# Kernel tuning notes

Measured on AMD Instinct MI355X. Metric: run time of the kernel, lower is better.

The kernel has to match this reference:

```python
import jax, jax.numpy as jnp
import numpy as np

N_NODES = 100000
N_EDGES = 1600000
N_GRAPHS = 4096
IN_DIM, HID, OUT_DIM = 128, 128, 64
BN_EPS = 1e-5


def gcn_conv(x, W, b, src, dst):
    """PyG GCNConv: symmetric norm with self-loops. x:[N,Fin] -> [N,Fout]."""
    h = x @ W  # [N, Fout]
    ones = jnp.ones((src.shape[0],), dtype=h.dtype)
    deg = jax.ops.segment_sum(ones, dst, num_segments=N_NODES) + 1.0  # +1 for self-loop
    dinv = jax.lax.rsqrt(deg)  # deg >= 1, safe
    norm = dinv[src] * dinv[dst]  # [E]
    msg = h[src] * norm[:, None]  # [E, Fout] gather + scale
    agg = jax.ops.segment_sum(msg, dst, num_segments=N_NODES)
    agg = agg + h * (dinv * dinv)[:, None]  # self-loop term, norm = dinv_i^2
    return agg + b


def batchnorm(x, gamma, beta):
    mu = jnp.mean(x, axis=0)
    var = jnp.mean(jnp.square(x - mu), axis=0)  # biased var, torch BN training mode
    return (x - mu) * jax.lax.rsqrt(var + BN_EPS) * gamma + beta


def setup_inputs() -> dict:
    key = jax.random.key(0)
    ks = jax.random.split(key, 12)
    x = jax.random.normal(ks[0], (N_NODES, IN_DIM), dtype=jnp.float32)
    edge_index = jax.random.randint(ks[1], (2, N_EDGES), 0, N_NODES, dtype=jnp.int64)
    batch = jnp.sort(jax.random.randint(ks[2], (N_NODES,), 0, N_GRAPHS, dtype=jnp.int64))
    def lin(k, fi, fo):
        s = 1.0 / np.sqrt(fi)
        return jax.random.uniform(k, (fi, fo), jnp.float32, -s, s)
    return {
        "x": x, "edge_index": edge_index, "batch": batch,
        "W1": lin(ks[3], IN_DIM, HID), "b1": jnp.zeros((HID,), jnp.float32),
        "g1": jnp.ones((HID,), jnp.float32), "be1": jnp.zeros((HID,), jnp.float32),
        "W2": lin(ks[4], HID, HID), "b2": jnp.zeros((HID,), jnp.float32),
        "g2": jnp.ones((HID,), jnp.float32), "be2": jnp.zeros((HID,), jnp.float32),
        "W3": lin(ks[5], HID, HID), "b3": jnp.zeros((HID,), jnp.float32),
        "g3": jnp.ones((HID,), jnp.float32), "be3": jnp.zeros((HID,), jnp.float32),
        "fcW": lin(ks[6], HID, OUT_DIM),
        "fcb": jax.random.uniform(ks[7], (OUT_DIM,), jnp.float32, -1/np.sqrt(HID), 1/np.sqrt(HID)),
    }


def reference(x, edge_index, batch, W1, b1, g1, be1, W2, b2, g2, be2, W3, b3, g3, be3, fcW, fcb):
    src, dst = edge_index[0], edge_index[1]
    h = jax.nn.relu(batchnorm(gcn_conv(x, W1, b1, src, dst), g1, be1))
    h = jax.nn.relu(batchnorm(gcn_conv(h, W2, b2, src, dst), g2, be2))
    h = jax.nn.relu(batchnorm(gcn_conv(h, W3, b3, src, dst), g3, be3))
    # global mean pool over graphs
    sums = jax.ops.segment_sum(h, batch, num_segments=N_GRAPHS)  # [G, HID]
    cnt = jax.ops.segment_sum(jnp.ones((N_NODES,), h.dtype), batch, num_segments=N_GRAPHS)
    pooled = sums / jnp.maximum(cnt, 1.0)[:, None]
    return pooled @ fcW + fcb
```

## Files before the change

kernel.cpp:

```cpp
#include <hip/hip_runtime.h>

#define NN 100000
#define NE 1600000
#define NG 4096
#define HID 128
#define ODIM 64
#define BN_EPS 1e-5f
#define NBUK 782
#define CHUNK 16384

typedef unsigned int u32;
typedef unsigned short u16;
typedef short short8 __attribute__((ext_vector_type(8)));
typedef float f32x4 __attribute__((ext_vector_type(4)));

__device__ inline u32 pack_bf16(float a, float b) {
  u32 ua = __float_as_uint(a), ub = __float_as_uint(b);
  ua += 0x7fffu + ((ua >> 16) & 1u);
  ub += 0x7fffu + ((ub >> 16) & 1u);
  return (ua >> 16) | (ub & 0xffff0000u);
}
__device__ inline u16 bf16_of(float v) {
  u32 ua = __float_as_uint(v);
  ua += 0x7fffu + ((ua >> 16) & 1u);
  return (u16)(ua >> 16);
}
__device__ inline float bf_lo(u32 u) { return __uint_as_float(u << 16); }
__device__ inline float bf_hi(u32 u) { return __uint_as_float(u & 0xffff0000u); }

__global__ __launch_bounds__(256) void k_bhist(const int* __restrict__ ei, int* __restrict__ bcnt) {
  __shared__ int h[NBUK];
  for (int i = threadIdx.x; i < NBUK; i += 256) h[i] = 0;
  __syncthreads();
  const int stride = 256 * 256;
  for (int e = blockIdx.x * 256 + threadIdx.x; e < NE; e += stride)
    atomicAdd(&h[ei[NE + e] >> 7], 1);
  __syncthreads();
  for (int i = threadIdx.x; i < NBUK; i += 256)
    if (h[i]) atomicAdd(&bcnt[i], h[i]);
}

__global__ __launch_bounds__(1024) void k_bscan(const int* __restrict__ bcnt, int* __restrict__ bboff,
                                                int* __restrict__ bcur, int* __restrict__ off) {
  __shared__ int ls[1024];
  int t = threadIdx.x;
  ls[t] = (t < NBUK) ? bcnt[t] : 0;
  __syncthreads();
  for (int d = 1; d < 1024; d <<= 1) {
    int v = 0;
    if (t >= d) v = ls[t - d];
    __syncthreads();
    ls[t] += v;
    __syncthreads();
  }
  if (t < NBUK) {
    int ex = (t == 0) ? 0 : ls[t - 1];
    bboff[t] = ex;
    bcur[t] = ex;
  }
  if (t == 0) { bboff[NBUK] = NE; off[NN] = NE; }
}

__global__ __launch_bounds__(1024) void k_bscatter(const int* __restrict__ ei, int* __restrict__ bcur,
                                                   u32* __restrict__ ebuf) {
  __shared__ int cnt[NBUK], rnk[NBUK], base[NBUK];
  int t = threadIdx.x;
  int e0 = blockIdx.x * CHUNK;
  for (int i = t; i < NBUK; i += 1024) { cnt[i] = 0; rnk[i] = 0; }
  __syncthreads();
  for (int i = t; i < CHUNK; i += 1024) {
    int e = e0 + i;
    if (e < NE) atomicAdd(&cnt[ei[NE + e] >> 7], 1);
  }
  __syncthreads();
  for (int i = t; i < NBUK; i += 1024) {
    int c = cnt[i];
    base[i] = c ? atomicAdd(&bcur[i], c) : 0;
  }
  __syncthreads();
  for (int i = t; i < CHUNK; i += 1024) {
    int e = e0 + i;
    if (e < NE) {
      int s = ei[e], d = ei[NE + e];
      int b = d >> 7;
      int r = atomicAdd(&rnk[b], 1);
      ebuf[base[b] + r] = ((u32)(d & 127) << 17) | (u32)s;
    }
  }
}

__global__ __launch_bounds__(256) void k_csr(const u32* __restrict__ ebuf, const int* __restrict__ bboff,
                                             int* __restrict__ off, float* __restrict__ dinv,
                                             u32* __restrict__ csrc) {
  __shared__ int cnt[128], base[128];
  int b = blockIdx.x, t = threadIdx.x;
  int n0 = b << 7;
  int ebeg = bboff[b], eend = bboff[b + 1];
  if (t < 128) cnt[t] = 0;
  __syncthreads();
  for (int e = ebeg + t; e < eend; e += 256) atomicAdd(&cnt[ebuf[e] >> 17], 1);
  __syncthreads();
  if (t < 128) base[t] = cnt[t];
  __syncthreads();
  for (int d = 1; d < 128; d <<= 1) {
    int v = 0;
    if (t >= d && t < 128) v = base[t - d];
    __syncthreads();
    if (t < 128) base[t] += v;
    __syncthreads();
  }
  int nvalid = min(128, NN - n0);
  if (t < 128) {
    int ex = base[t] - cnt[t];
    base[t] = ex;
    if (t < nvalid) {
      off[n0 + t] = ebeg + ex;
      dinv[n0 + t] = rsqrtf((float)cnt[t] + 1.0f);
    }
  }
  __syncthreads();
  for (int e = ebeg + t; e < eend; e += 256) {
    u32 p = ebuf[e];
    int d = p >> 17;
    int pos = ebeg + atomicAdd(&base[d], 1);
    csrc[pos] = p & 0x1ffffu;
  }
}

__global__ __launch_bounds__(256) void k_goff(const int* __restrict__ batch, int* __restrict__ goff) {
  int g = blockIdx.x * 256 + threadIdx.x;
  if (g > NG) return;
  int lo = 0, hi = NN;
  while (lo < hi) { int mid = (lo + hi) >> 1; if (batch[mid] < g) lo = mid + 1; else hi = mid; }
  goff[g] = lo;
}

__global__ __launch_bounds__(128) void k_wprep(const float* __restrict__ W, u16* __restrict__ Wt) {
  int n = blockIdx.x, k = threadIdx.x;
  Wt[(size_t)n * HID + k] = bf16_of(W[(size_t)k * HID + n]);
}

__global__ __launch_bounds__(256) void k_gemm1(const float* __restrict__ A, const u16* __restrict__ Wt,
                                               const float* __restrict__ dinv, u16* __restrict__ H) {
  __shared__ u16 Ct[128][128];
  u16 (*At)[32] = (u16 (*)[32])(&Ct[0][0]);
  u16 (*Bt)[32] = (u16 (*)[32])(&Ct[32][0]);

  int t = threadIdx.x;
  int w = t >> 6, l = t & 63;
  int quad = l >> 4, lid = l & 15;
  int row0 = blockIdx.x * 128;

  f32x4 acc[2][8];
#pragma unroll
  for (int mt = 0; mt < 2; ++mt)
#pragma unroll
    for (int nt = 0; nt < 8; ++nt) acc[mt][nt] = (f32x4){0.f, 0.f, 0.f, 0.f};

  int ar = t >> 1;
  int ac = (t & 1) << 4;
  int grow = row0 + ar;
  bool aok = grow < NN;

  for (int k0 = 0; k0 < HID; k0 += 32) {
    float4 f0 = {0, 0, 0, 0}, f1 = {0, 0, 0, 0}, f2 = {0, 0, 0, 0}, f3 = {0, 0, 0, 0};
    if (aok) {
      const float4* ap = (const float4*)(A + (size_t)grow * HID + k0 + ac);
      f0 = ap[0]; f1 = ap[1]; f2 = ap[2]; f3 = ap[3];
    }
    uint4 q0, q1;
    q0.x = pack_bf16(f0.x, f0.y); q0.y = pack_bf16(f0.z, f0.w);
    q0.z = pack_bf16(f1.x, f1.y); q0.w = pack_bf16(f1.z, f1.w);
    q1.x = pack_bf16(f2.x, f2.y); q1.y = pack_bf16(f2.z, f2.w);
    q1.z = pack_bf16(f3.x, f3.y); q1.w = pack_bf16(f3.z, f3.w);
    *(uint4*)&At[ar][ac] = q0;
    *(uint4*)&At[ar][ac + 8] = q1;
    const u16* wp = Wt + (size_t)(t >> 1) * HID + k0 + ac;
    *(uint4*)&Bt[t >> 1][ac]     = ((const uint4*)wp)[0];
    *(uint4*)&Bt[t >> 1][ac + 8] = ((const uint4*)wp)[1];
    __syncthreads();
    short8 a0 = *(const short8*)&At[(w << 5) + lid][quad << 3];
    short8 a1 = *(const short8*)&At[(w << 5) + 16 + lid][quad << 3];
#pragma unroll
    for (int nt = 0; nt < 8; ++nt) {
      short8 b = *(const short8*)&Bt[(nt << 4) + lid][quad << 3];
      acc[0][nt] = __builtin_amdgcn_mfma_f32_16x16x32_bf16(a0, b, acc[0][nt], 0, 0, 0);
      acc[1][nt] = __builtin_amdgcn_mfma_f32_16x16x32_bf16(a1, b, acc[1][nt], 0, 0, 0);
    }
    __syncthreads();
  }

  int valid = min(128, NN - row0);
#pragma unroll
  for (int mt = 0; mt < 2; ++mt) {
#pragma unroll
    for (int r = 0; r < 4; ++r) {
      int rl = (w << 5) + (mt << 4) + (quad << 2) + r;
      float dv = (rl < valid) ? dinv[row0 + rl] : 0.f;
#pragma unroll
      for (int nt = 0; nt < 8; ++nt) {
        Ct[rl][(nt << 4) + lid] = bf16_of(acc[mt][nt][r] * dv);
      }
    }
  }
  __syncthreads();
  u16* Hb = H + (size_t)row0 * HID;
  int tot = valid << 4;
  for (int idx = t; idx < tot; idx += 256) {
    ((uint4*)Hb)[idx] = ((const uint4*)Ct)[idx];
  }
}

__device__ inline u32 bn_pair(u32 v, float2 sc, float2 sh) {
  float a = fmaxf(fmaf(bf_lo(v), sc.x, sh.x), 0.f);
  float b = fmaxf(fmaf(bf_hi(v), sc.y, sh.y), 0.f);
  return pack_bf16(a, b);
}

__global__ __launch_bounds__(256) void k_gemm_b(const u16* __restrict__ A, const u16* __restrict__ Wt,
                                                const float* __restrict__ scale, const float* __restrict__ shift,
                                                const float* __restrict__ dinv, u16* __restrict__ H) {
  __shared__ u16 Ct[128][128];
  u16 (*At)[32] = (u16 (*)[32])(&Ct[0][0]);
  u16 (*Bt)[32] = (u16 (*)[32])(&Ct[32][0]);

  int t = threadIdx.x;
  int w = t >> 6, l = t & 63;
  int quad = l >> 4, lid = l & 15;
  int row0 = blockIdx.x * 128;

  f32x4 acc[2][8];
#pragma unroll
  for (int mt = 0; mt < 2; ++mt)
#pragma unroll
    for (int nt = 0; nt < 8; ++nt) acc[mt][nt] = (f32x4){0.f, 0.f, 0.f, 0.f};

  int ar = t >> 1;
  int ac = (t & 1) << 4;
  int grow = row0 + ar;
  bool aok = grow < NN;

  for (int k0 = 0; k0 < HID; k0 += 32) {
    uint4 q0 = {0, 0, 0, 0}, q1 = {0, 0, 0, 0};
    if (aok) {
      const uint4* ap = (const uint4*)(A + (size_t)grow * HID + k0 + ac);
      q0 = ap[0]; q1 = ap[1];
    }
    const float2* scp = (const float2*)(scale + k0 + ac);
    const float2* shp = (const float2*)(shift + k0 + ac);
    q0.x = bn_pair(q0.x, scp[0], shp[0]); q0.y = bn_pair(q0.y, scp[1], shp[1]);
    q0.z = bn_pair(q0.z, scp[2], shp[2]); q0.w = bn_pair(q0.w, scp[3], shp[3]);
    q1.x = bn_pair(q1.x, scp[4], shp[4]); q1.y = bn_pair(q1.y, scp[5], shp[5]);
    q1.z = bn_pair(q1.z, scp[6], shp[6]); q1.w = bn_pair(q1.w, scp[7], shp[7]);
    *(uint4*)&At[ar][ac] = q0;
    *(uint4*)&At[ar][ac + 8] = q1;
    const u16* wp = Wt + (size_t)(t >> 1) * HID + k0 + ac;
    *(uint4*)&Bt[t >> 1][ac]     = ((const uint4*)wp)[0];
    *(uint4*)&Bt[t >> 1][ac + 8] = ((const uint4*)wp)[1];
    __syncthreads();
    short8 a0 = *(const short8*)&At[(w << 5) + lid][quad << 3];
    short8 a1 = *(const short8*)&At[(w << 5) + 16 + lid][quad << 3];
#pragma unroll
    for (int nt = 0; nt < 8; ++nt) {
      short8 b = *(const short8*)&Bt[(nt << 4) + lid][quad << 3];
      acc[0][nt] = __builtin_amdgcn_mfma_f32_16x16x32_bf16(a0, b, acc[0][nt], 0, 0, 0);
      acc[1][nt] = __builtin_amdgcn_mfma_f32_16x16x32_bf16(a1, b, acc[1][nt], 0, 0, 0);
    }
    __syncthreads();
  }

  int valid = min(128, NN - row0);
#pragma unroll
  for (int mt = 0; mt < 2; ++mt) {
#pragma unroll
    for (int r = 0; r < 4; ++r) {
      int rl = (w << 5) + (mt << 4) + (quad << 2) + r;
      float dv = (rl < valid) ? dinv[row0 + rl] : 0.f;
#pragma unroll
      for (int nt = 0; nt < 8; ++nt) {
        Ct[rl][(nt << 4) + lid] = bf16_of(acc[mt][nt][r] * dv);
      }
    }
  }
  __syncthreads();
  u16* Hb = H + (size_t)row0 * HID;
  int tot = valid << 4;
  for (int idx = t; idx < tot; idx += 256) {
    ((uint4*)Hb)[idx] = ((const uint4*)Ct)[idx];
  }
}

__global__ __launch_bounds__(256) void k_agg(const u16* __restrict__ h2, const int* __restrict__ off,
                                             const u32* __restrict__ csrc, const float* __restrict__ dinv,
                                             u16* __restrict__ aggb) {
  int node = (int)((blockIdx.x * 256 + threadIdx.x) >> 6);
  int lane = threadIdx.x & 63;
  if (node >= NN) return;
  int beg = off[node], end = off[node + 1];
  u32 us = ((const u32*)(h2 + (size_t)node * HID))[lane];
  float ax = bf_lo(us), ay = bf_hi(us);
  int e = beg;
  for (; e + 4 <= end; e += 4) {
    u32 s0 = csrc[e], s1 = csrc[e + 1], s2 = csrc[e + 2], s3 = csrc[e + 3];
    u32 v0 = ((const u32*)(h2 + (size_t)s0 * HID))[lane];
    u32 v1 = ((const u32*)(h2 + (size_t)s1 * HID))[lane];
    u32 v2 = ((const u32*)(h2 + (size_t)s2 * HID))[lane];
    u32 v3 = ((const u32*)(h2 + (size_t)s3 * HID))[lane];
    ax += bf_lo(v0) + bf_lo(v1) + bf_lo(v2) + bf_lo(v3);
    ay += bf_hi(v0) + bf_hi(v1) + bf_hi(v2) + bf_hi(v3);
  }
  for (; e < end; ++e) {
    u32 v = ((const u32*)(h2 + (size_t)csrc[e] * HID))[lane];
    ax += bf_lo(v);
    ay += bf_hi(v);
  }
  float di = dinv[node];
  ((u32*)(aggb + (size_t)node * HID))[lane] = pack_bf16(ax * di, ay * di);
}

__global__ __launch_bounds__(256) void k_bnstats(const u16* __restrict__ X, float* __restrict__ buf) {
  __shared__ float lsx[256], lssx[256], lsy[256], lssy[256];
  int t = threadIdx.x;
  int colp = t & 63, grp = t >> 6;
  int rbeg = blockIdx.x * 256, rend = min(rbeg + 256, NN);
  float sx = 0.f, ssx = 0.f, sy = 0.f, ssy = 0.f;
  for (int r = rbeg + grp; r < rend; r += 4) {
    u32 v = ((const u32*)(X + (size_t)r * HID))[colp];
    float a = bf_lo(v), b = bf_hi(v);
    sx += a; ssx = fmaf(a, a, ssx);
    sy += b; ssy = fmaf(b, b, ssy);
  }
  lsx[t] = sx; lssx[t] = ssx; lsy[t] = sy; lssy[t] = ssy;
  __syncthreads();
  if (t < 64) {
    sx = lsx[t] + lsx[t + 64] + lsx[t + 128] + lsx[t + 192];
    ssx = lssx[t] + lssx[t + 64] + lssx[t + 128] + lssx[t + 192];
    sy = lsy[t] + lsy[t + 64] + lsy[t + 128] + lsy[t + 192];
    ssy = lssy[t] + lssy[t + 64] + lssy[t + 128] + lssy[t + 192];
    atomicAdd(&buf[2 * colp], sx);
    atomicAdd(&buf[2 * colp + 1], sy);
    atomicAdd(&buf[HID + 2 * colp], ssx);
    atomicAdd(&buf[HID + 2 * colp + 1], ssy);
  }
}

__global__ void k_bnfinal(float* __restrict__ buf, const float* __restrict__ g, const float* __restrict__ be) {
  int j = threadIdx.x;
  const float invN = 1.0f / (float)NN;
  float mu = buf[j] * invN;
  float var = buf[HID + j] * invN - mu * mu;
  float sc = g[j] * rsqrtf(var + BN_EPS);
  buf[j] = sc;
  buf[HID + j] = be[j] - mu * sc;
}

__global__ __launch_bounds__(256) void k_pool(const u16* __restrict__ aggb, const float* __restrict__ bn,
                                              const int* __restrict__ goff, float* __restrict__ pooled) {
  int g = (int)((blockIdx.x * 256 + threadIdx.x) >> 6);
  int lane = threadIdx.x & 63;
  if (g >= NG) return;
  int beg = goff[g], end = goff[g + 1];
  float2 sc = ((const float2*)bn)[lane];
  float2 sh = ((const float2*)(bn + HID))[lane];
  float2 acc; acc.x = 0.f; acc.y = 0.f;
  for (int r = beg; r < end; ++r) {
    u32 v = ((const u32*)(aggb + (size_t)r * HID))[lane];
    acc.x += fmaxf(fmaf(bf_lo(v), sc.x, sh.x), 0.f);
    acc.y += fmaxf(fmaf(bf_hi(v), sc.y, sh.y), 0.f);
  }
  float inv = 1.0f / fmaxf((float)(end - beg), 1.0f);
  acc.x *= inv; acc.y *= inv;
  ((float2*)(pooled + (size_t)g * HID))[lane] = acc;
}

__global__ __launch_bounds__(256) void k_fc(const float* __restrict__ pooled, const float* __restrict__ fcW,
                                            const float* __restrict__ fcb, float* __restrict__ out) {
  int t = threadIdx.x;
  int c = t & 63;
  int g = blockIdx.x * 4 + (t >> 6);
  if (g >= NG) return;
  const float* p = pooled + (size_t)g * HID;
  float acc = fcb[c];
#pragma unroll 8
  for (int k = 0; k < HID; ++k) acc = fmaf(p[k], fcW[(size_t)k * ODIM + c], acc);
  out[(size_t)g * ODIM + c] = acc;
}

extern "C" void kernel_launch(void* const* d_in, const int* in_sizes, int n_in,
                              void* d_out, int out_size, void* d_ws, size_t ws_size,
                              hipStream_t stream) {
  const float* x     = (const float*)d_in[0];
  const int*   ei    = (const int*)d_in[1];
  const int*   batch = (const int*)d_in[2];
  const float* W1    = (const float*)d_in[3];
  const float* g1    = (const float*)d_in[5];
  const float* be1   = (const float*)d_in[6];
  const float* W2    = (const float*)d_in[7];
  const float* g2    = (const float*)d_in[9];
  const float* be2   = (const float*)d_in[10];
  const float* W3    = (const float*)d_in[11];
  const float* g3    = (const float*)d_in[13];
  const float* be3   = (const float*)d_in[14];
  const float* fcW   = (const float*)d_in[15];
  const float* fcb   = (const float*)d_in[16];
  float* out = (float*)d_out;

  char* p = (char*)d_ws;
  auto alloc = [&](size_t bytes) { char* r = p; p += (bytes + 255) & ~(size_t)255; return r; };
  int*   bcnt   = (int*)alloc((size_t)NBUK * 4);
  float* bnb    = (float*)alloc(3 * 256 * 4);
  size_t zbytes = (size_t)(p - (char*)d_ws);
  int*   bboff  = (int*)alloc((size_t)(NBUK + 1) * 4);
  int*   bcur   = (int*)alloc((size_t)NBUK * 4);
  int*   off    = (int*)alloc((size_t)(NN + 1) * 4);
  float* dinv   = (float*)alloc((size_t)NN * 4);
  u32*   ebuf   = (u32*)alloc((size_t)NE * 4);
  u32*   csrc   = (u32*)alloc((size_t)NE * 4);
  int*   goff   = (int*)alloc((size_t)(NG + 1) * 4);
  u16*   Wt1    = (u16*)alloc((size_t)HID * HID * 2);
  u16*   Wt2    = (u16*)alloc((size_t)HID * HID * 2);
  u16*   Wt3    = (u16*)alloc((size_t)HID * HID * 2);
  u16*   h2     = (u16*)alloc((size_t)NN * HID * 2);
  u16*   aggb   = (u16*)alloc((size_t)NN * HID * 2);
  float* pooled = (float*)alloc((size_t)NG * HID * 4);

  hipMemsetAsync(d_ws, 0, zbytes, stream);

  const int NB = (NN + 255) / 256;
  const int GB = (NN + 127) / 128;
  const int AGB = NN / 4;
  const int SB = (NE + CHUNK - 1) / CHUNK;

  k_bhist<<<256, 256, 0, stream>>>(ei, bcnt);
  k_bscan<<<1, 1024, 0, stream>>>(bcnt, bboff, bcur, off);
  k_bscatter<<<SB, 1024, 0, stream>>>(ei, bcur, ebuf);
  k_csr<<<NBUK, 256, 0, stream>>>(ebuf, bboff, off, dinv, csrc);
  k_goff<<<(NG + 1 + 255) / 256, 256, 0, stream>>>(batch, goff);
  k_wprep<<<HID, HID, 0, stream>>>(W1, Wt1);
  k_wprep<<<HID, HID, 0, stream>>>(W2, Wt2);
  k_wprep<<<HID, HID, 0, stream>>>(W3, Wt3);

  k_gemm1<<<GB, 256, 0, stream>>>(x, Wt1, dinv, h2);
  k_agg<<<AGB, 256, 0, stream>>>(h2, off, csrc, dinv, aggb);
  k_bnstats<<<NB, 256, 0, stream>>>(aggb, bnb);
  k_bnfinal<<<1, 128, 0, stream>>>(bnb, g1, be1);
  k_gemm_b<<<GB, 256, 0, stream>>>(aggb, Wt2, bnb, bnb + HID, dinv, h2);
  k_agg<<<AGB, 256, 0, stream>>>(h2, off, csrc, dinv, aggb);
  k_bnstats<<<NB, 256, 0, stream>>>(aggb, bnb + 256);
  k_bnfinal<<<1, 128, 0, stream>>>(bnb + 256, g2, be2);
  k_gemm_b<<<GB, 256, 0, stream>>>(aggb, Wt3, bnb + 256, bnb + 256 + HID, dinv, h2);
  k_agg<<<AGB, 256, 0, stream>>>(h2, off, csrc, dinv, aggb);
  k_bnstats<<<NB, 256, 0, stream>>>(aggb, bnb + 512);
  k_bnfinal<<<1, 128, 0, stream>>>(bnb + 512, g3, be3);
  k_pool<<<(NG * 64) / 256, 256, 0, stream>>>(aggb, bnb + 512, goff, pooled);
  k_fc<<<NG / 4, 256, 0, stream>>>(pooled, fcW, fcb, out);
}
```

Before: 582.0 us.

## Fuse prep, BN finalize, and pool+FC kernels to cut launch count

Merges the edge histogram, graph offset search and three weight transposes into one multi-role prep kernel. Folds the BN finalize step into each consumer: gemm_b computes scale and shift into shared memory, and the pool kernel computes them per lane. Fuses mean pooling with the final FC layer through shared memory, which drops the pooled buffer. This removes about nine small kernel launches and their gaps, at the cost of redundant BN-finalize arithmetic in every block.

```diff
diff --git a/kernel.cpp b/kernel.cpp
--- a/kernel.cpp
+++ b/kernel.cpp
@@ -8,6 +8,9 @@
 #define BN_EPS 1e-5f
 #define NBUK 782
 #define CHUNK 16384
+#define PREP_HIST 256
+#define PREP_GOFF 17
+#define PREP_W 192
 
 typedef unsigned int u32;
 typedef unsigned short u16;
@@ -28,16 +31,38 @@
 __device__ inline float bf_lo(u32 u) { return __uint_as_float(u << 16); }
 __device__ inline float bf_hi(u32 u) { return __uint_as_float(u & 0xffff0000u); }
 
-__global__ __launch_bounds__(256) void k_bhist(const int* __restrict__ ei, int* __restrict__ bcnt) {
+__global__ __launch_bounds__(256) void k_prep(const int* __restrict__ ei, int* __restrict__ bcnt,
+                                              const int* __restrict__ batch, int* __restrict__ goff,
+                                              const float* __restrict__ W1, const float* __restrict__ W2,
+                                              const float* __restrict__ W3, u16* __restrict__ Wt1,
+                                              u16* __restrict__ Wt2, u16* __restrict__ Wt3) {
   __shared__ int h[NBUK];
-  for (int i = threadIdx.x; i < NBUK; i += 256) h[i] = 0;
-  __syncthreads();
-  const int stride = 256 * 256;
-  for (int e = blockIdx.x * 256 + threadIdx.x; e < NE; e += stride)
-    atomicAdd(&h[ei[NE + e] >> 7], 1);
-  __syncthreads();
-  for (int i = threadIdx.x; i < NBUK; i += 256)
-    if (h[i]) atomicAdd(&bcnt[i], h[i]);
+  int b = blockIdx.x, t = threadIdx.x;
+  if (b < PREP_HIST) {
+    for (int i = t; i < NBUK; i += 256) h[i] = 0;
+    __syncthreads();
+    const int stride = PREP_HIST * 256;
+    for (int e = b * 256 + t; e < NE; e += stride)
+      atomicAdd(&h[ei[NE + e] >> 7], 1);
+    __syncthreads();
+    for (int i = t; i < NBUK; i += 256)
+      if (h[i]) atomicAdd(&bcnt[i], h[i]);
+  } else if (b < PREP_HIST + PREP_GOFF) {
+    int g = (b - PREP_HIST) * 256 + t;
+    if (g <= NG) {
+      int lo = 0, hi = NN;
+      while (lo < hi) { int mid = (lo + hi) >> 1; if (batch[mid] < g) lo = mid + 1; else hi = mid; }
+      goff[g] = lo;
+    }
+  } else {
+    int idx = (b - PREP_HIST - PREP_GOFF) * 256 + t;
+    int mat = idx >> 14;
+    int rem = idx & 16383;
+    int n = rem >> 7, k = rem & 127;
+    const float* W = (mat == 0) ? W1 : (mat == 1) ? W2 : W3;
+    u16* Wt = (mat == 0) ? Wt1 : (mat == 1) ? Wt2 : Wt3;
+    Wt[(n << 7) + k] = bf16_of(W[(k << 7) + n]);
+  }
 }
 
 __global__ __launch_bounds__(1024) void k_bscan(const int* __restrict__ bcnt, int* __restrict__ bboff,
@@ -125,19 +150,6 @@
     int pos = ebeg + atomicAdd(&base[d], 1);
     csrc[pos] = p & 0x1ffffu;
   }
-}
-
-__global__ __launch_bounds__(256) void k_goff(const int* __restrict__ batch, int* __restrict__ goff) {
-  int g = blockIdx.x * 256 + threadIdx.x;
-  if (g > NG) return;
-  int lo = 0, hi = NN;
-  while (lo < hi) { int mid = (lo + hi) >> 1; if (batch[mid] < g) lo = mid + 1; else hi = mid; }
-  goff[g] = lo;
-}
-
-__global__ __launch_bounds__(128) void k_wprep(const float* __restrict__ W, u16* __restrict__ Wt) {
-  int n = blockIdx.x, k = threadIdx.x;
-  Wt[(size_t)n * HID + k] = bf16_of(W[(size_t)k * HID + n]);
 }
 
 __global__ __launch_bounds__(256) void k_gemm1(const float* __restrict__ A, const u16* __restrict__ Wt,
@@ -218,16 +230,27 @@
 }
 
 __global__ __launch_bounds__(256) void k_gemm_b(const u16* __restrict__ A, const u16* __restrict__ Wt,
-                                                const float* __restrict__ scale, const float* __restrict__ shift,
+                                                const float* __restrict__ sums, const float* __restrict__ g,
+                                                const float* __restrict__ be,
                                                 const float* __restrict__ dinv, u16* __restrict__ H) {
   __shared__ u16 Ct[128][128];
   u16 (*At)[32] = (u16 (*)[32])(&Ct[0][0]);
   u16 (*Bt)[32] = (u16 (*)[32])(&Ct[32][0]);
+  float* scsh = (float*)&Ct[64][0];
 
   int t = threadIdx.x;
   int w = t >> 6, l = t & 63;
   int quad = l >> 4, lid = l & 15;
   int row0 = blockIdx.x * 128;
+
+  if (t < 128) {
+    const float invN = 1.0f / (float)NN;
+    float mu = sums[t] * invN;
+    float var = sums[HID + t] * invN - mu * mu;
+    float sc = g[t] * rsqrtf(var + BN_EPS);
+    scsh[t] = sc;
+    scsh[128 + t] = be[t] - mu * sc;
+  }
 
   f32x4 acc[2][8];
 #pragma unroll
@@ -239,6 +262,7 @@
   int ac = (t & 1) << 4;
   int grow = row0 + ar;
   bool aok = grow < NN;
+  __syncthreads();
 
   for (int k0 = 0; k0 < HID; k0 += 32) {
     uint4 q0 = {0, 0, 0, 0}, q1 = {0, 0, 0, 0};
@@ -246,8 +270,8 @@
       const uint4* ap = (const uint4*)(A + (size_t)grow * HID + k0 + ac);
       q0 = ap[0]; q1 = ap[1];
     }
-    const float2* scp = (const float2*)(scale + k0 + ac);
-    const float2* shp = (const float2*)(shift + k0 + ac);
+    const float2* scp = (const float2*)(scsh + k0 + ac);
+    const float2* shp = (const float2*)(scsh + 128 + k0 + ac);
     q0.x = bn_pair(q0.x, scp[0], shp[0]); q0.y = bn_pair(q0.y, scp[1], shp[1]);
     q0.z = bn_pair(q0.z, scp[2], shp[2]); q0.w = bn_pair(q0.w, scp[3], shp[3]);
     q1.x = bn_pair(q1.x, scp[4], shp[4]); q1.y = bn_pair(q1.y, scp[5], shp[5]);
@@ -344,46 +368,36 @@
   }
 }
 
-__global__ void k_bnfinal(float* __restrict__ buf, const float* __restrict__ g, const float* __restrict__ be) {
-  int j = threadIdx.x;
+__global__ __launch_bounds__(256) void k_poolfc(const u16* __restrict__ aggb, const float* __restrict__ sums,
+                                                const float* __restrict__ g3, const float* __restrict__ be3,
+                                                const int* __restrict__ goff, const float* __restrict__ fcW,
+                                                const float* __restrict__ fcb, float* __restrict__ out) {
+  __shared__ float ls[4][128];
+  int t = threadIdx.x;
+  int w = t >> 6, lane = t & 63;
+  int gr = blockIdx.x * 4 + w;
   const float invN = 1.0f / (float)NN;
-  float mu = buf[j] * invN;
-  float var = buf[HID + j] * invN - mu * mu;
-  float sc = g[j] * rsqrtf(var + BN_EPS);
-  buf[j] = sc;
-  buf[HID + j] = be[j] - mu * sc;
-}
-
-__global__ __launch_bounds__(256) void k_pool(const u16* __restrict__ aggb, const float* __restrict__ bn,
-                                              const int* __restrict__ goff, float* __restrict__ pooled) {
-  int g = (int)((blockIdx.x * 256 + threadIdx.x) >> 6);
-  int lane = threadIdx.x & 63;
-  if (g >= NG) return;
-  int beg = goff[g], end = goff[g + 1];
-  float2 sc = ((const float2*)bn)[lane];
-  float2 sh = ((const float2*)(bn + HID))[lane];
-  float2 acc; acc.x = 0.f; acc.y = 0.f;
+  int f0 = lane << 1, f1 = f0 + 1;
+  float mu0 = sums[f0] * invN, mu1 = sums[f1] * invN;
+  float v0 = sums[HID + f0] * invN - mu0 * mu0;
+  float v1 = sums[HID + f1] * invN - mu1 * mu1;
+  float sc0 = g3[f0] * rsqrtf(v0 + BN_EPS), sc1 = g3[f1] * rsqrtf(v1 + BN_EPS);
+  float sh0 = be3[f0] - mu0 * sc0, sh1 = be3[f1] - mu1 * sc1;
+  int beg = goff[gr], end = goff[gr + 1];
+  float ax = 0.f, ay = 0.f;
   for (int r = beg; r < end; ++r) {
     u32 v = ((const u32*)(aggb + (size_t)r * HID))[lane];
-    acc.x += fmaxf(fmaf(bf_lo(v), sc.x, sh.x), 0.f);
-    acc.y += fmaxf(fmaf(bf_hi(v), sc.y, sh.y), 0.f);
+    ax += fmaxf(fmaf(bf_lo(v), sc0, sh0), 0.f);
+    ay += fmaxf(fmaf(bf_hi(v), sc1, sh1), 0.f);
   }
   float inv = 1.0f / fmaxf((float)(end - beg), 1.0f);
-  acc.x *= inv; acc.y *= inv;
-  ((float2*)(pooled + (size_t)g * HID))[lane] = acc;
-}
-
-__global__ __launch_bounds__(256) void k_fc(const float* __restrict__ pooled, const float* __restrict__ fcW,
-                                            const float* __restrict__ fcb, float* __restrict__ out) {
-  int t = threadIdx.x;
-  int c = t & 63;
-  int g = blockIdx.x * 4 + (t >> 6);
-  if (g >= NG) return;
-  const float* p = pooled + (size_t)g * HID;
-  float acc = fcb[c];
+  ls[w][f0] = ax * inv;
+  ls[w][f1] = ay * inv;
+  __syncthreads();
+  float acc = fcb[lane];
 #pragma unroll 8
-  for (int k = 0; k < HID; ++k) acc = fmaf(p[k], fcW[(size_t)k * ODIM + c], acc);
-  out[(size_t)g * ODIM + c] = acc;
+  for (int k = 0; k < HID; ++k) acc = fmaf(ls[w][k], fcW[(size_t)k * ODIM + lane], acc);
+  out[(size_t)gr * ODIM + lane] = acc;
 }
 
 extern "C" void kernel_launch(void* const* d_in, const int* in_sizes, int n_in,
@@ -422,7 +436,6 @@
   u16*   Wt3    = (u16*)alloc((size_t)HID * HID * 2);
   u16*   h2     = (u16*)alloc((size_t)NN * HID * 2);
   u16*   aggb   = (u16*)alloc((size_t)NN * HID * 2);
-  float* pooled = (float*)alloc((size_t)NG * HID * 4);
 
   hipMemsetAsync(d_ws, 0, zbytes, stream);
 
@@ -431,27 +444,19 @@
   const int AGB = NN / 4;
   const int SB = (NE + CHUNK - 1) / CHUNK;
 
-  k_bhist<<<256, 256, 0, stream>>>(ei, bcnt);
+  k_prep<<<PREP_HIST + PREP_GOFF + PREP_W, 256, 0, stream>>>(ei, bcnt, batch, goff, W1, W2, W3, Wt1, Wt2, Wt3);
   k_bscan<<<1, 1024, 0, stream>>>(bcnt, bboff, bcur, off);
   k_bscatter<<<SB, 1024, 0, stream>>>(ei, bcur, ebuf);
   k_csr<<<NBUK, 256, 0, stream>>>(ebuf, bboff, off, dinv, csrc);
-  k_goff<<<(NG + 1 + 255) / 256, 256, 0, stream>>>(batch, goff);
-  k_wprep<<<HID, HID, 0, stream>>>(W1, Wt1);
-  k_wprep<<<HID, HID, 0, stream>>>(W2, Wt2);
-  k_wprep<<<HID, HID, 0, stream>>>(W3, Wt3);
 
   k_gemm1<<<GB, 256, 0, stream>>>(x, Wt1, dinv, h2);
   k_agg<<<AGB, 256, 0, stream>>>(h2, off, csrc, dinv, aggb);
   k_bnstats<<<NB, 256, 0, stream>>>(aggb, bnb);
-  k_bnfinal<<<1, 128, 0, stream>>>(bnb, g1, be1);
-  k_gemm_b<<<GB, 256, 0, stream>>>(aggb, Wt2, bnb, bnb + HID, dinv, h2);
+  k_gemm_b<<<GB, 256, 0, stream>>>(aggb, Wt2, bnb, g1, be1, dinv, h2);
   k_agg<<<AGB, 256, 0, stream>>>(h2, off, csrc, dinv, aggb);
   k_bnstats<<<NB, 256, 0, stream>>>(aggb, bnb + 256);
-  k_bnfinal<<<1, 128, 0, stream>>>(bnb + 256, g2, be2);
-  k_gemm_b<<<GB, 256, 0, stream>>>(aggb, Wt3, bnb + 256, bnb + 256 + HID, dinv, h2);
+  k_gemm_b<<<GB, 256, 0, stream>>>(aggb, Wt3, bnb + 256, g2, be2, dinv, h2);
   k_agg<<<AGB, 256, 0, stream>>>(h2, off, csrc, dinv, aggb);
   k_bnstats<<<NB, 256, 0, stream>>>(aggb, bnb + 512);
-  k_bnfinal<<<1, 128, 0, stream>>>(bnb + 512, g3, be3);
-  k_pool<<<(NG * 64) / 256, 256, 0, stream>>>(aggb, bnb + 512, goff, pooled);
-  k_fc<<<NG / 4, 256, 0, stream>>>(pooled, fcW, fcb, out);
-}
+  k_poolfc<<<NG / 4, 256, 0, stream>>>(aggb, bnb + 512, g3, be3, goff, fcW, fcb, out);
+}
```

After: 555.1 us. 1.05x faster.
